# Performance work log

Measured on AMD Instinct MI355X. Metric: run time of the kernel, lower is better.

## Reference

```python
import jax, jax.numpy as jnp
import numpy as np

B, S, D = 2, 2048, 1024
H = 16
DH = D // H  # 64

def setup_inputs() -> dict:
    key = jax.random.key(0)
    ks = jax.random.split(key, 7)
    sc = 1.0 / np.sqrt(DH)
    return {
        "sequences": jax.random.normal(ks[0], (B, S, D), dtype=jnp.float32),
        "Wq": jax.random.normal(ks[1], (H, DH, DH), dtype=jnp.float32) * sc,
        "bq": jax.random.normal(ks[2], (H, DH), dtype=jnp.float32) * 0.02,
        "Wk": jax.random.normal(ks[3], (H, DH, DH), dtype=jnp.float32) * sc,
        "bk": jax.random.normal(ks[4], (H, DH), dtype=jnp.float32) * 0.02,
        "Wv": jax.random.normal(ks[5], (H, DH, DH), dtype=jnp.float32) * sc,
        "bv": jax.random.normal(ks[6], (H, DH), dtype=jnp.float32) * 0.02,
    }

def reference(sequences, Wq, bq, Wk, bk, Wv, bv):
    b, s, _ = sequences.shape
    x = sequences.reshape(b, s, H, DH)  # [B,S,H,Dh]
    # torch Linear: y = x @ W^T + b; W is [out,in] => einsum contracts input dim d
    q = jnp.einsum("bshd,hed->bshe", x, Wq) + bq  # [B,S,H,Dh]
    k = jnp.einsum("bshd,hed->bshe", x, Wk) + bk
    v = jnp.einsum("bshd,hed->bshe", x, Wv) + bv
    scores = jnp.einsum("bshd,bthd->bhst", q, k) / jnp.sqrt(jnp.float32(DH))
    attn = jax.nn.softmax(scores, axis=-1)  # [B,H,S,S]
    out = jnp.einsum("bhst,bthd->bshd", attn, v)  # [B,S,H,Dh]
    return out.reshape(b, s, H * DH)
```

## Files before the change

### kernel.cpp

```cpp
#include <hip/hip_runtime.h>

typedef unsigned short u16;
typedef unsigned int   u32;
typedef __bf16 bf16x8 __attribute__((ext_vector_type(8)));
typedef float  f32x4  __attribute__((ext_vector_type(4)));
typedef float  f32x16 __attribute__((ext_vector_type(16)));
typedef u16    u16x4  __attribute__((ext_vector_type(4)));
typedef u32    u32x4  __attribute__((ext_vector_type(4)));

#define HH   16
#define DHH  64
#define SEQL 2048
#define NB   2
#define BHN  (NB * HH)
#define SCLF 0.1803368801111204f
#define KVB  128
#define NT   (SEQL / KVB)

static __device__ __forceinline__ u16 f2bf(float f) {
    return __builtin_bit_cast(u16, (__bf16)f);
}
static __device__ __forceinline__ u32 pack2(float a, float b) {
    return (u32)f2bf(a) | ((u32)f2bf(b) << 16);
}
static __device__ __forceinline__ void plswap(u32 &a, u32 &b) {
    asm volatile("v_permlane32_swap_b32 %0, %1" : "+v"(a), "+v"(b));
}

static __device__ __forceinline__ void gload_lds16(const void* g, void* l) {
    __builtin_amdgcn_global_load_lds(
        (const __attribute__((address_space(1))) unsigned int*)g,
        (__attribute__((address_space(3))) unsigned int*)l, 16, 0, 0);
}

__global__ __launch_bounds__(256) void wconv_kernel(
    const float* __restrict__ Wq, const float* __restrict__ Wk,
    const float* __restrict__ Wv, u16* __restrict__ Wb)
{
    const int m = blockIdx.y;
    const float* W = (m == 0) ? Wq : (m == 1) ? Wk : Wv;
    const float s = (m == 0) ? SCLF : 1.0f;
    const int i = (blockIdx.x * 256 + threadIdx.x) * 4;
    float4 v = *reinterpret_cast<const float4*>(W + i);
    u16x4 o = { f2bf(v.x * s), f2bf(v.y * s), f2bf(v.z * s), f2bf(v.w * s) };
    *reinterpret_cast<u16x4*>(Wb + (size_t)m * 65536 + i) = o;
}

__global__ __launch_bounds__(256) void qkv_kernel(
    const float* __restrict__ x, const u16* __restrict__ Wb,
    const float* __restrict__ bq, const float* __restrict__ bk,
    const float* __restrict__ bv,
    u16* __restrict__ Qws, u16* __restrict__ Kws, u16* __restrict__ Vtws)
{
    const int h   = blockIdx.y;
    const int r0  = blockIdx.x * 64;
    const int tid = threadIdx.x;
    const int w   = tid >> 6;
    const int l   = tid & 63;
    const int c   = l & 15;
    const int g   = l >> 4;

    __shared__ u16 vt[64 * 72];

    bf16x8 xa[2];
    {
        const float* xp = x + (size_t)(r0 + w * 16 + c) * 1024 + h * 64 + g * 8;
        #pragma unroll
        for (int kh = 0; kh < 2; ++kh) {
            float4 lo = *reinterpret_cast<const float4*>(xp + kh * 32);
            float4 hi = *reinterpret_cast<const float4*>(xp + kh * 32 + 4);
            bf16x8 f;
            f[0]=(__bf16)lo.x; f[1]=(__bf16)lo.y; f[2]=(__bf16)lo.z; f[3]=(__bf16)lo.w;
            f[4]=(__bf16)hi.x; f[5]=(__bf16)hi.y; f[6]=(__bf16)hi.z; f[7]=(__bf16)hi.w;
            xa[kh] = f;
        }
    }

    const int b      = r0 >> 11;
    const int s_base = r0 & (SEQL - 1);
    const int bh     = b * HH + h;

    const float* bs[3] = {bq + h * 64, bk + h * 64, bv + h * 64};

    #pragma unroll
    for (int m = 0; m < 3; ++m) {
        const u16*   W    = Wb + (size_t)m * 65536 + h * 4096;
        const float* bias = bs[m];
        const float  bscl = (m == 0) ? SCLF : 1.0f;
        f32x4 acc[4];
        #pragma unroll
        for (int ct = 0; ct < 4; ++ct) {
            acc[ct][0] = 0.f; acc[ct][1] = 0.f; acc[ct][2] = 0.f; acc[ct][3] = 0.f;
        }
        #pragma unroll
        for (int kh = 0; kh < 2; ++kh) {
            #pragma unroll
            for (int ct = 0; ct < 4; ++ct) {
                bf16x8 wf = *reinterpret_cast<const bf16x8*>(
                    W + (ct * 16 + c) * 64 + kh * 32 + g * 8);
                acc[ct] = __builtin_amdgcn_mfma_f32_16x16x32_bf16(xa[kh], wf, acc[ct], 0, 0, 0);
            }
        }
        if (m < 2) {
            if (m == 1) __syncthreads();
            #pragma unroll
            for (int ct = 0; ct < 4; ++ct) {
                float bb = bias[ct * 16 + c] * bscl;
                #pragma unroll
                for (int r = 0; r < 4; ++r)
                    vt[(w * 16 + g * 4 + r) * 72 + ct * 16 + c] = f2bf(acc[ct][r] + bb);
            }
            __syncthreads();
            {
                const int d  = tid >> 2;
                const int s0 = (tid & 3) * 16;
                u16* outp = (m == 0 ? Qws : Kws) +
                            ((size_t)bh * SEQL + s_base + d) * 64 + s0;
                uint4 v0 = *reinterpret_cast<const uint4*>(&vt[d * 72 + s0]);
                uint4 v1 = *reinterpret_cast<const uint4*>(&vt[d * 72 + s0 + 8]);
                *reinterpret_cast<uint4*>(outp)     = v0;
                *reinterpret_cast<uint4*>(outp + 8) = v1;
            }
        } else {
            __syncthreads();
            #pragma unroll
            for (int ct = 0; ct < 4; ++ct) {
                float bb = bias[ct * 16 + c];
                u16x4 pb;
                #pragma unroll
                for (int r = 0; r < 4; ++r)
                    pb[r] = f2bf(acc[ct][r] + bb);
                *reinterpret_cast<u16x4*>(&vt[(ct * 16 + c) * 72 + w * 16 + g * 4]) = pb;
            }
            __syncthreads();
            {
                const int d  = tid >> 2;
                const int s0 = (tid & 3) * 16;
                u16* vp = Vtws + ((size_t)bh * 64 + d) * SEQL + s_base + s0;
                uint4 v0 = *reinterpret_cast<const uint4*>(&vt[d * 72 + s0]);
                uint4 v1 = *reinterpret_cast<const uint4*>(&vt[d * 72 + s0 + 8]);
                *reinterpret_cast<uint4*>(vp)     = v0;
                *reinterpret_cast<uint4*>(vp + 8) = v1;
            }
        }
    }
}

__global__ __launch_bounds__(256, 2) void attn_kernel(
    const u16* __restrict__ Qws, const u16* __restrict__ Kws,
    const u16* __restrict__ Vtws, float* __restrict__ out)
{
    const int p     = blockIdx.x;
    const int lid   = (p & 7) * 64 + (p >> 3);
    const int qtile = lid & 15;
    const int bh    = lid >> 4;
    const int b     = bh >> 4;
    const int h     = bh & 15;

    const int tid = threadIdx.x;
    const int w   = tid >> 6;
    const int l   = tid & 63;
    const int lq  = l & 31;
    const int hi  = l >> 5;
    const int q0  = qtile * 128 + w * 32;

    __shared__ u16 k_lds[2][KVB * 64];
    __shared__ u16 v_lds[2][64 * KVB];

    const u16* Kb = Kws  + (size_t)bh * SEQL * 64;
    const u16* Vb = Vtws + (size_t)bh * 64 * SEQL;

    #define STAGE(bb, k0)                                                     \
    {   const int rs8 = l >> 3, c8 = l & 7;                                   \
        _Pragma("unroll")                                                     \
        for (int a = 0; a < 4; ++a) {                                         \
            const int rbase = w * 32 + a * 8;                                 \
            gload_lds16(Kb + (size_t)((k0) + rbase + rs8) * 64 + (c8 ^ rs8) * 8, \
                        &k_lds[bb][rbase * 64]);                              \
        }                                                                     \
        const int rs16 = l >> 4, c16 = l & 15;                                \
        _Pragma("unroll")                                                     \
        for (int a = 0; a < 4; ++a) {                                         \
            const int rbase = w * 16 + a * 4;                                 \
            const int sxv   = c16 ^ ((a * 4 + rs16) & 15);                    \
            gload_lds16(Vb + (size_t)(rbase + rs16) * SEQL + (k0) + sxv * 8,  \
                        &v_lds[bb][rbase * KVB]);                             \
        }                                                                     \
    }

    bf16x8 qf[4];
    #pragma unroll
    for (int s = 0; s < 4; ++s)
        qf[s] = *reinterpret_cast<const bf16x8*>(
            Qws + ((size_t)bh * SEQL + q0 + lq) * 64 + s * 16 + hi * 8);

    f32x16 zero16;
    #pragma unroll
    for (int j = 0; j < 16; ++j) zero16[j] = 0.f;

    f32x16 acc[2];
    acc[0] = zero16; acc[1] = zero16;
    float mrow = -1e30f;
    float lrow = 0.f;

    int koff[4];
    #pragma unroll
    for (int s = 0; s < 4; ++s) koff[s] = ((s * 2 + hi) ^ (lq & 7)) * 16;

    bf16x8 vfA[2][4], vfB[2][4];
    bf16x8 pfA[4], pfB[4];

    STAGE(0, 0);
    __syncthreads();

    auto subbody = [&](bf16x8 (&vfC)[2][4], bf16x8 (&pfC)[4],
                       bf16x8 (&vfP)[2][4], bf16x8 (&pfP)[4],
                       int cur, int ks, bool has_prev) {
        const char* kb = reinterpret_cast<const char*>(&k_lds[cur][0]) + ks * (64 * 128);
        bf16x8 kf0[4], kf1[4];
        #pragma unroll
        for (int s = 0; s < 4; ++s) {
            kf0[s] = *reinterpret_cast<const bf16x8*>(kb + lq * 128 + koff[s]);
            kf1[s] = *reinterpret_cast<const bf16x8*>(kb + (32 + lq) * 128 + koff[s]);
        }

        __builtin_amdgcn_s_setprio(1);
        f32x16 st0 = __builtin_amdgcn_mfma_f32_32x32x16_bf16(kf0[0], qf[0], zero16, 0, 0, 0);
        f32x16 st1 = __builtin_amdgcn_mfma_f32_32x32x16_bf16(kf1[0], qf[0], zero16, 0, 0, 0);
        #pragma unroll
        for (int s = 1; s < 4; ++s) {
            st0 = __builtin_amdgcn_mfma_f32_32x32x16_bf16(kf0[s], qf[s], st0, 0, 0, 0);
            st1 = __builtin_amdgcn_mfma_f32_32x32x16_bf16(kf1[s], qf[s], st1, 0, 0, 0);
        }
        if (has_prev) {
            #pragma unroll
            for (int s = 0; s < 4; ++s) {
                acc[0] = __builtin_amdgcn_mfma_f32_32x32x16_bf16(vfP[0][s], pfP[s], acc[0], 0, 0, 0);
                acc[1] = __builtin_amdgcn_mfma_f32_32x32x16_bf16(vfP[1][s], pfP[s], acc[1], 0, 0, 0);
            }
        }
        __builtin_amdgcn_s_setprio(0);

        const char* vb = reinterpret_cast<const char*>(&v_lds[cur][0]);
        #pragma unroll
        for (int dt = 0; dt < 2; ++dt)
            #pragma unroll
            for (int s = 0; s < 4; ++s) {
                const int slot = (ks * 8 + s * 2 + hi) ^ (lq & 15);
                vfC[dt][s] = *reinterpret_cast<const bf16x8*>(
                    vb + (dt * 32 + lq) * 256 + slot * 16);
            }

        float t0 = fmaxf(fmaxf(st0[0], st0[1]),  fmaxf(st0[2], st0[3]));
        float t1 = fmaxf(fmaxf(st0[4], st0[5]),  fmaxf(st0[6], st0[7]));
        float t2 = fmaxf(fmaxf(st0[8], st0[9]),  fmaxf(st0[10], st0[11]));
        float t3 = fmaxf(fmaxf(st0[12], st0[13]), fmaxf(st0[14], st0[15]));
        float t4 = fmaxf(fmaxf(st1[0], st1[1]),  fmaxf(st1[2], st1[3]));
        float t5 = fmaxf(fmaxf(st1[4], st1[5]),  fmaxf(st1[6], st1[7]));
        float t6 = fmaxf(fmaxf(st1[8], st1[9]),  fmaxf(st1[10], st1[11]));
        float t7 = fmaxf(fmaxf(st1[12], st1[13]), fmaxf(st1[14], st1[15]));
        float mx = fmaxf(fmaxf(fmaxf(t0, t1), fmaxf(t2, t3)),
                         fmaxf(fmaxf(t4, t5), fmaxf(t6, t7)));
        mx = fmaxf(mx, __shfl_xor(mx, 32, 64));

        if (!__all(mx <= mrow + 8.f)) {
            const float mn    = fmaxf(mrow, mx);
            const float alpha = __builtin_amdgcn_exp2f(mrow - mn);
            mrow = mn;
            lrow *= alpha;
            #pragma unroll
            for (int j = 0; j < 16; ++j) { acc[0][j] *= alpha; acc[1][j] *= alpha; }
        }

        float rs0 = 0.f, rs1 = 0.f;
        u32 wd[16];
        {
            float pp[16];
            #pragma unroll
            for (int r = 0; r < 16; ++r) {
                pp[r] = __builtin_amdgcn_exp2f(st0[r] - mrow);
                if (r & 1) rs1 += pp[r]; else rs0 += pp[r];
            }
            #pragma unroll
            for (int j = 0; j < 8; ++j) wd[j] = pack2(pp[2 * j], pp[2 * j + 1]);
        }
        {
            float pp[16];
            #pragma unroll
            for (int r = 0; r < 16; ++r) {
                pp[r] = __builtin_amdgcn_exp2f(st1[r] - mrow);
                if (r & 1) rs1 += pp[r]; else rs0 += pp[r];
            }
            #pragma unroll
            for (int j = 0; j < 8; ++j) wd[8 + j] = pack2(pp[2 * j], pp[2 * j + 1]);
        }
        lrow += rs0 + rs1;

        plswap(wd[0],  wd[2]);  plswap(wd[1],  wd[3]);
        plswap(wd[4],  wd[6]);  plswap(wd[5],  wd[7]);
        plswap(wd[8],  wd[10]); plswap(wd[9],  wd[11]);
        plswap(wd[12], wd[14]); plswap(wd[13], wd[15]);

        #pragma unroll
        for (int s = 0; s < 4; ++s) {
            u32x4 tmp = { wd[s * 4 + 0], wd[s * 4 + 1], wd[s * 4 + 2], wd[s * 4 + 3] };
            pfC[s] = __builtin_bit_cast(bf16x8, tmp);
        }
    };

    for (int t = 0; t < NT; ++t) {
        const int cur = t & 1;
        if (t + 1 < NT) STAGE(cur ^ 1, (t + 1) * KVB);
        subbody(vfA, pfA, vfB, pfB, cur, 0, t != 0);
        subbody(vfB, pfB, vfA, pfA, cur, 1, true);
        __syncthreads();
    }

    #pragma unroll
    for (int s = 0; s < 4; ++s) {
        acc[0] = __builtin_amdgcn_mfma_f32_32x32x16_bf16(vfB[0][s], pfB[s], acc[0], 0, 0, 0);
        acc[1] = __builtin_amdgcn_mfma_f32_32x32x16_bf16(vfB[1][s], pfB[s], acc[1], 0, 0, 0);
    }
    const float inv = 1.f / (lrow + __shfl_xor(lrow, 32, 64));

    float* op = out + ((size_t)b * SEQL + q0 + lq) * 1024 + h * 64 + hi * 4;
    #pragma unroll
    for (int dt = 0; dt < 2; ++dt)
        #pragma unroll
        for (int rg = 0; rg < 4; ++rg) {
            float4 o;
            o.x = acc[dt][rg * 4 + 0] * inv;
            o.y = acc[dt][rg * 4 + 1] * inv;
            o.z = acc[dt][rg * 4 + 2] * inv;
            o.w = acc[dt][rg * 4 + 3] * inv;
            *reinterpret_cast<float4*>(op + dt * 32 + rg * 8) = o;
        }
}

extern "C" void kernel_launch(void* const* d_in, const int* in_sizes, int n_in,
                              void* d_out, int out_size, void* d_ws, size_t ws_size,
                              hipStream_t stream) {
    const float* x  = (const float*)d_in[0];
    const float* Wq = (const float*)d_in[1];
    const float* bq = (const float*)d_in[2];
    const float* Wk = (const float*)d_in[3];
    const float* bk = (const float*)d_in[4];
    const float* Wv = (const float*)d_in[5];
    const float* bv = (const float*)d_in[6];
    float* out = (float*)d_out;

    const size_t per = (size_t)BHN * SEQL * 64;
    u16* Qws = (u16*)d_ws;
    u16* Kws = Qws + per;
    u16* Vt  = Kws + per;
    u16* Wb  = Vt  + per;

    wconv_kernel<<<dim3(64, 3), 256, 0, stream>>>(Wq, Wk, Wv, Wb);
    qkv_kernel<<<dim3(64, 16), 256, 0, stream>>>(x, Wb, bq, bk, bv, Qws, Kws, Vt);
    attn_kernel<<<dim3(512), 256, 0, stream>>>(Qws, Kws, Vt, out);
}
```

Measured before the change: 87.92 us.

## Split KV range into two independent online-softmax streams merged at the end

Each tile now loads 64 keys from the first half of the sequence and 64 from the second half, and keeps two separate softmax states (max, sum, accumulator) that are merged in the epilogue. This replaces the previous software pipeline, where PV for one subtile overlapped QK of the next, with two independent dependency chains the scheduler can interleave. It costs extra accumulator registers, which may reduce occupancy, and adds a final rescale-and-combine step.

```diff
diff --git a/kernel.cpp b/kernel.cpp
--- a/kernel.cpp
+++ b/kernel.cpp
@@ -15,7 +15,7 @@
 #define BHN  (NB * HH)
 #define SCLF 0.1803368801111204f
 #define KVB  128
-#define NT   (SEQL / KVB)
+#define NT   16
 
 static __device__ __forceinline__ u16 f2bf(float f) {
     return __builtin_bit_cast(u16, (__bf16)f);
@@ -170,12 +170,13 @@
     const u16* Kb = Kws  + (size_t)bh * SEQL * 64;
     const u16* Vb = Vtws + (size_t)bh * 64 * SEQL;
 
-    #define STAGE(bb, k0)                                                     \
+    #define STAGE(bb, k0A, k0B)                                               \
     {   const int rs8 = l >> 3, c8 = l & 7;                                   \
+        const int kbw = (w < 2) ? (k0A) : ((k0B) - 64);                       \
         _Pragma("unroll")                                                     \
         for (int a = 0; a < 4; ++a) {                                         \
             const int rbase = w * 32 + a * 8;                                 \
-            gload_lds16(Kb + (size_t)((k0) + rbase + rs8) * 64 + (c8 ^ rs8) * 8, \
+            gload_lds16(Kb + (size_t)(kbw + rbase + rs8) * 64 + (c8 ^ rs8) * 8, \
                         &k_lds[bb][rbase * 64]);                              \
         }                                                                     \
         const int rs16 = l >> 4, c16 = l & 15;                                \
@@ -183,7 +184,9 @@
         for (int a = 0; a < 4; ++a) {                                         \
             const int rbase = w * 16 + a * 4;                                 \
             const int sxv   = c16 ^ ((a * 4 + rs16) & 15);                    \
-            gload_lds16(Vb + (size_t)(rbase + rs16) * SEQL + (k0) + sxv * 8,  \
+            const int kk    = (sxv < 8) ? ((k0A) + sxv * 8)                   \
+                                        : ((k0B) + (sxv - 8) * 8);            \
+            gload_lds16(Vb + (size_t)(rbase + rs16) * SEQL + kk,              \
                         &v_lds[bb][rbase * KVB]);                             \
         }                                                                     \
     }
@@ -198,59 +201,19 @@
     #pragma unroll
     for (int j = 0; j < 16; ++j) zero16[j] = 0.f;
 
-    f32x16 acc[2];
-    acc[0] = zero16; acc[1] = zero16;
-    float mrow = -1e30f;
-    float lrow = 0.f;
+    f32x16 accA[2], accB[2];
+    accA[0] = zero16; accA[1] = zero16;
+    accB[0] = zero16; accB[1] = zero16;
+    float mrowA = -1e30f, lrowA = 0.f;
+    float mrowB = -1e30f, lrowB = 0.f;
 
     int koff[4];
     #pragma unroll
     for (int s = 0; s < 4; ++s) koff[s] = ((s * 2 + hi) ^ (lq & 7)) * 16;
 
-    bf16x8 vfA[2][4], vfB[2][4];
-    bf16x8 pfA[4], pfB[4];
-
-    STAGE(0, 0);
-    __syncthreads();
-
-    auto subbody = [&](bf16x8 (&vfC)[2][4], bf16x8 (&pfC)[4],
-                       bf16x8 (&vfP)[2][4], bf16x8 (&pfP)[4],
-                       int cur, int ks, bool has_prev) {
-        const char* kb = reinterpret_cast<const char*>(&k_lds[cur][0]) + ks * (64 * 128);
-        bf16x8 kf0[4], kf1[4];
-        #pragma unroll
-        for (int s = 0; s < 4; ++s) {
-            kf0[s] = *reinterpret_cast<const bf16x8*>(kb + lq * 128 + koff[s]);
-            kf1[s] = *reinterpret_cast<const bf16x8*>(kb + (32 + lq) * 128 + koff[s]);
-        }
-
-        __builtin_amdgcn_s_setprio(1);
-        f32x16 st0 = __builtin_amdgcn_mfma_f32_32x32x16_bf16(kf0[0], qf[0], zero16, 0, 0, 0);
-        f32x16 st1 = __builtin_amdgcn_mfma_f32_32x32x16_bf16(kf1[0], qf[0], zero16, 0, 0, 0);
-        #pragma unroll
-        for (int s = 1; s < 4; ++s) {
-            st0 = __builtin_amdgcn_mfma_f32_32x32x16_bf16(kf0[s], qf[s], st0, 0, 0, 0);
-            st1 = __builtin_amdgcn_mfma_f32_32x32x16_bf16(kf1[s], qf[s], st1, 0, 0, 0);
-        }
-        if (has_prev) {
-            #pragma unroll
-            for (int s = 0; s < 4; ++s) {
-                acc[0] = __builtin_amdgcn_mfma_f32_32x32x16_bf16(vfP[0][s], pfP[s], acc[0], 0, 0, 0);
-                acc[1] = __builtin_amdgcn_mfma_f32_32x32x16_bf16(vfP[1][s], pfP[s], acc[1], 0, 0, 0);
-            }
-        }
-        __builtin_amdgcn_s_setprio(0);
-
-        const char* vb = reinterpret_cast<const char*>(&v_lds[cur][0]);
-        #pragma unroll
-        for (int dt = 0; dt < 2; ++dt)
-            #pragma unroll
-            for (int s = 0; s < 4; ++s) {
-                const int slot = (ks * 8 + s * 2 + hi) ^ (lq & 15);
-                vfC[dt][s] = *reinterpret_cast<const bf16x8*>(
-                    vb + (dt * 32 + lq) * 256 + slot * 16);
-            }
-
+    auto smax = [&](const f32x16& st0, const f32x16& st1,
+                    float& mrow, float& lrow, f32x16 (&acc)[2],
+                    bf16x8 (&pf)[4]) {
         float t0 = fmaxf(fmaxf(st0[0], st0[1]),  fmaxf(st0[2], st0[3]));
         float t1 = fmaxf(fmaxf(st0[4], st0[5]),  fmaxf(st0[6], st0[7]));
         float t2 = fmaxf(fmaxf(st0[8], st0[9]),  fmaxf(st0[10], st0[11]));
@@ -304,24 +267,98 @@
         #pragma unroll
         for (int s = 0; s < 4; ++s) {
             u32x4 tmp = { wd[s * 4 + 0], wd[s * 4 + 1], wd[s * 4 + 2], wd[s * 4 + 3] };
-            pfC[s] = __builtin_bit_cast(bf16x8, tmp);
+            pf[s] = __builtin_bit_cast(bf16x8, tmp);
         }
     };
+
+    STAGE(0, 0, 1024);
+    __syncthreads();
 
     for (int t = 0; t < NT; ++t) {
         const int cur = t & 1;
-        if (t + 1 < NT) STAGE(cur ^ 1, (t + 1) * KVB);
-        subbody(vfA, pfA, vfB, pfB, cur, 0, t != 0);
-        subbody(vfB, pfB, vfA, pfA, cur, 1, true);
+        if (t + 1 < NT) STAGE(cur ^ 1, (t + 1) * 64, 1024 + (t + 1) * 64);
+
+        const char* kb = reinterpret_cast<const char*>(&k_lds[cur][0]);
+        const char* vb = reinterpret_cast<const char*>(&v_lds[cur][0]);
+
+        f32x16 sA0, sA1, sB0, sB1;
+        __builtin_amdgcn_s_setprio(1);
+        {
+            bf16x8 k0[4], k1[4];
+            #pragma unroll
+            for (int s = 0; s < 4; ++s) {
+                k0[s] = *reinterpret_cast<const bf16x8*>(kb + lq * 128 + koff[s]);
+                k1[s] = *reinterpret_cast<const bf16x8*>(kb + (32 + lq) * 128 + koff[s]);
+            }
+            sA0 = __builtin_amdgcn_mfma_f32_32x32x16_bf16(k0[0], qf[0], zero16, 0, 0, 0);
+            sA1 = __builtin_amdgcn_mfma_f32_32x32x16_bf16(k1[0], qf[0], zero16, 0, 0, 0);
+            #pragma unroll
+            for (int s = 1; s < 4; ++s) {
+                sA0 = __builtin_amdgcn_mfma_f32_32x32x16_bf16(k0[s], qf[s], sA0, 0, 0, 0);
+                sA1 = __builtin_amdgcn_mfma_f32_32x32x16_bf16(k1[s], qf[s], sA1, 0, 0, 0);
+            }
+        }
+        {
+            bf16x8 k0[4], k1[4];
+            #pragma unroll
+            for (int s = 0; s < 4; ++s) {
+                k0[s] = *reinterpret_cast<const bf16x8*>(kb + (64 + lq) * 128 + koff[s]);
+                k1[s] = *reinterpret_cast<const bf16x8*>(kb + (96 + lq) * 128 + koff[s]);
+            }
+            sB0 = __builtin_amdgcn_mfma_f32_32x32x16_bf16(k0[0], qf[0], zero16, 0, 0, 0);
+            sB1 = __builtin_amdgcn_mfma_f32_32x32x16_bf16(k1[0], qf[0], zero16, 0, 0, 0);
+            #pragma unroll
+            for (int s = 1; s < 4; ++s) {
+                sB0 = __builtin_amdgcn_mfma_f32_32x32x16_bf16(k0[s], qf[s], sB0, 0, 0, 0);
+                sB1 = __builtin_amdgcn_mfma_f32_32x32x16_bf16(k1[s], qf[s], sB1, 0, 0, 0);
+            }
+        }
+        __builtin_amdgcn_s_setprio(0);
+
+        bf16x8 vfA[2][4], vfB[2][4];
+        #pragma unroll
+        for (int dt = 0; dt < 2; ++dt)
+            #pragma unroll
+            for (int s = 0; s < 4; ++s) {
+                const int sa = (s * 2 + hi) ^ (lq & 15);
+                const int sb = (8 + s * 2 + hi) ^ (lq & 15);
+                vfA[dt][s] = *reinterpret_cast<const bf16x8*>(
+                    vb + (dt * 32 + lq) * 256 + sa * 16);
+                vfB[dt][s] = *reinterpret_cast<const bf16x8*>(
+                    vb + (dt * 32 + lq) * 256 + sb * 16);
+            }
+
+        bf16x8 pfA[4];
+        smax(sA0, sA1, mrowA, lrowA, accA, pfA);
+
+        __builtin_amdgcn_s_setprio(1);
+        #pragma unroll
+        for (int s = 0; s < 4; ++s) {
+            accA[0] = __builtin_amdgcn_mfma_f32_32x32x16_bf16(vfA[0][s], pfA[s], accA[0], 0, 0, 0);
+            accA[1] = __builtin_amdgcn_mfma_f32_32x32x16_bf16(vfA[1][s], pfA[s], accA[1], 0, 0, 0);
+        }
+        __builtin_amdgcn_s_setprio(0);
+
+        bf16x8 pfB[4];
+        smax(sB0, sB1, mrowB, lrowB, accB, pfB);
+
+        __builtin_amdgcn_s_setprio(1);
+        #pragma unroll
+        for (int s = 0; s < 4; ++s) {
+            accB[0] = __builtin_amdgcn_mfma_f32_32x32x16_bf16(vfB[0][s], pfB[s], accB[0], 0, 0, 0);
+            accB[1] = __builtin_amdgcn_mfma_f32_32x32x16_bf16(vfB[1][s], pfB[s], accB[1], 0, 0, 0);
+        }
+        __builtin_amdgcn_s_setprio(0);
+
         __syncthreads();
     }
 
-    #pragma unroll
-    for (int s = 0; s < 4; ++s) {
-        acc[0] = __builtin_amdgcn_mfma_f32_32x32x16_bf16(vfB[0][s], pfB[s], acc[0], 0, 0, 0);
-        acc[1] = __builtin_amdgcn_mfma_f32_32x32x16_bf16(vfB[1][s], pfB[s], acc[1], 0, 0, 0);
-    }
-    const float inv = 1.f / (lrow + __shfl_xor(lrow, 32, 64));
+    const float mn = fmaxf(mrowA, mrowB);
+    const float aA = __builtin_amdgcn_exp2f(mrowA - mn);
+    const float aB = __builtin_amdgcn_exp2f(mrowB - mn);
+    const float lA = lrowA + __shfl_xor(lrowA, 32, 64);
+    const float lB = lrowB + __shfl_xor(lrowB, 32, 64);
+    const float inv = 1.f / (lA * aA + lB * aB);
 
     float* op = out + ((size_t)b * SEQL + q0 + lq) * 1024 + h * 64 + hi * 4;
     #pragma unroll
@@ -329,10 +366,10 @@
         #pragma unroll
         for (int rg = 0; rg < 4; ++rg) {
             float4 o;
-            o.x = acc[dt][rg * 4 + 0] * inv;
-            o.y = acc[dt][rg * 4 + 1] * inv;
-            o.z = acc[dt][rg * 4 + 2] * inv;
-            o.w = acc[dt][rg * 4 + 3] * inv;
+            #pragma unroll
+            for (int j = 0; j < 4; ++j)
+                ((float*)&o)[j] = (accA[dt][rg * 4 + j] * aA +
+                                   accB[dt][rg * 4 + j] * aB) * inv;
             *reinterpret_cast<float4*>(op + dt * 32 + rg * 8) = o;
         }
 }
```

Measured after the change: 102.0 us. 1.16x slower.
